# Performance work log

Hardware: AMD Instinct MI355X
Metric: run time of the kernel (lower is better)

The kernel has to match this reference:

```python
import jax, jax.numpy as jnp
import numpy as np

B, N, D = 8, 2048, 256
K = 3  # conv kernel size

def causal_conv(x, w, b):
    # x: [B, N, D] -> conv over seq with left replicate padding (causal)
    xc = jnp.transpose(x, (0, 2, 1))                       # [B, D, N]
    xc = jnp.pad(xc, ((0, 0), (0, 0), (K - 1, 0)), mode='edge')
    y = jax.lax.conv_general_dilated(
        xc, w, window_strides=(1,), padding='VALID',
        dimension_numbers=('NCH', 'OIH', 'NCH'))           # [B, Dout, N]
    y = y + b[None, :, None]
    return jnp.transpose(y, (0, 2, 1))                     # [B, N, Dout]

def setup_inputs() -> dict:
    key = jax.random.key(0)
    ks = jax.random.split(key, 5)
    query = jax.random.normal(ks[0], (B, N, D), dtype=jnp.float32)
    keys = jax.random.normal(ks[1], (B, N, D), dtype=jnp.float32)
    vals = jax.random.normal(ks[2], (B, N, D), dtype=jnp.float32)
    # causal mask [B, N, N]: attend to positions j <= i
    mask = jnp.broadcast_to(jnp.tril(jnp.ones((N, N), dtype=jnp.int32)), (B, N, N))
    conv_w = jax.random.normal(ks[3], (D, D, K), dtype=jnp.float32) * (1.0 / np.sqrt(D * K))
    conv_b = jnp.zeros((D,), dtype=jnp.float32)
    return {"query": query, "keys": keys, "vals": vals, "mask": mask,
            "conv_w": conv_w, "conv_b": conv_b}

def reference(query, keys, vals, mask, conv_w, conv_b):
    q = causal_conv(query, conv_w, conv_b)                 # [B, N, D]
    k = causal_conv(keys, conv_w, conv_b)                  # [B, N, D]
    # Euclidean pairwise distances: ||q_i - k_j||
    q2 = jnp.sum(q * q, axis=-1)                           # [B, N]
    k2 = jnp.sum(k * k, axis=-1)                           # [B, N]
    qk = jnp.einsum('bid,bjd->bij', q, k)                  # [B, N, N]
    d2 = jnp.maximum(q2[:, :, None] + k2[:, None, :] - 2.0 * qk, 0.0)
    distances = jnp.sqrt(d2)
    presoftmax = jnp.where(mask == 0, -jnp.inf, -distances)
    attn = jax.nn.softmax(presoftmax, axis=-1)             # [B, N, N]
    shifted_vals = jnp.roll(vals, shift=1, axis=1).at[:, 0, :].set(0.0)
    return jnp.einsum('bij,bjd->bid', attn, shifted_vals)  # [B, N, D]
```

## Files before the change

kernel.cpp:

```cpp
#include <hip/hip_runtime.h>

typedef _Float16 f16;
typedef _Float16 f16x4 __attribute__((ext_vector_type(4)));
typedef _Float16 f16x8 __attribute__((ext_vector_type(8)));
typedef float f32x4 __attribute__((ext_vector_type(4)));

#define NB 8
#define NS 2048
#define ND 256
#define NM (NB * NS)
#define LOG2E 1.44269504f


__device__ __forceinline__ int swzK(int row, int col) {
  return (((row) << 9) | ((col) << 1)) ^ (((row) & 7) << 4);
}

__global__ __launch_bounds__(256) void prep_kernel(
    const float* __restrict__ vals, const float* __restrict__ conv_w,
    f16* __restrict__ vT, f16* __restrict__ Wk) {
  int tid = threadIdx.x;
  if (blockIdx.x < 512) {
    __shared__ f16 Vl[32 * 256];
    int tile = blockIdx.x;
    for (int s = tid; s < 1024; s += 256) {
      int j = s >> 5, d0 = (s & 31) * 8;
      int g = tile * 32 + j;
      f16x8 h;
      if ((g & (NS - 1)) == 0) {
        for (int e = 0; e < 8; e++) h[e] = (f16)0.f;
      } else {
        const float* src = vals + (size_t)(g - 1) * ND + d0;
        f32x4 v0 = *(const f32x4*)src, v1 = *(const f32x4*)(src + 4);
        for (int e = 0; e < 4; e++) { h[e] = (f16)v0[e]; h[4 + e] = (f16)v1[e]; }
      }
      *(f16x8*)((char*)Vl + j * 512 + d0 * 2) = h;
    }
    __syncthreads();
    char* dst = (char*)vT + (size_t)tile * 16384;
    #pragma unroll
    for (int k = 0; k < 4; k++) {
      int ch = tid + k * 256;
      int lane = ch & 63;
      int d = ((ch >> 6) << 4) + (lane & 15);
      int g4c = lane >> 4;
      f16x8 h;
      #pragma unroll
      for (int js = 0; js < 2; js++)
        #pragma unroll
        for (int r = 0; r < 4; r++)
          h[js * 4 + r] = *(const f16*)((const char*)Vl + (js * 16 + 4 * g4c + r) * 512 + d * 2);
      *(f16x8*)(dst + ch * 16) = h;
    }
  } else {
    int e = (blockIdx.x - 512) * 256 + tid;
    if (e < 256 * 768) {
      int o = e / 768, kk = e - o * 768;
      int tap = kk >> 8, d = kk & 255;
      Wk[e] = (f16)conv_w[o * 768 + d * 3 + tap];
    }
  }
}

__global__ __launch_bounds__(256) void conv_kernel(
    const float* __restrict__ query, const float* __restrict__ keys,
    const float* __restrict__ bias, const f16* __restrict__ Wk,
    f16* __restrict__ qT, f16* __restrict__ kT,
    float* __restrict__ q2, float* __restrict__ k2) {
  __shared__ f16 Xl[66 * 256];
  __shared__ float red[4][64];
  int bid = blockIdx.x;
  int tens = bid >> 8;
  int tile = bid & 255;
  const float* X = tens ? keys : query;
  float* Y2 = tens ? k2 : q2;
  int base = tile * 64;
  int bstart = base & ~(NS - 1);
  int tid = threadIdx.x;
  for (int c = tid; c < 66 * 32; c += 256) {
    int row = c >> 5, d0 = (c & 31) * 8;
    int g = base - 2 + row; if (g < bstart) g = bstart;
    const float* src = X + (size_t)g * ND + d0;
    f32x4 v0 = *(const f32x4*)src, v1 = *(const f32x4*)(src + 4);
    f16x8 h;
    for (int e = 0; e < 4; e++) { h[e] = (f16)v0[e]; h[4 + e] = (f16)v1[e]; }
    *(f16x8*)((char*)Xl + swzK(row, d0)) = h;
  }
  __syncthreads();
  int lane = tid & 63, w = tid >> 6;
  int c16 = lane & 15, g4 = lane >> 4;
  f32x4 acc[4][4] = {};
  const f16* wbase = Wk + (size_t)(w * 64 + c16) * 768 + 8 * g4;
  f16x8 bcur[4], bnext[4];
  #pragma unroll
  for (int nt = 0; nt < 4; nt++) bcur[nt] = *(const f16x8*)(wbase + nt * 16 * 768);
  for (int ks = 0; ks < 24; ks++) {
    int kk0 = ks * 32;
    if (ks < 23) {
      #pragma unroll
      for (int nt = 0; nt < 4; nt++)
        bnext[nt] = *(const f16x8*)(wbase + nt * 16 * 768 + kk0 + 32);
    }
    int tap = kk0 >> 8, d0 = kk0 & 255;
    f16x8 afr[4];
    #pragma unroll
    for (int ms = 0; ms < 4; ms++)
      afr[ms] = *(const f16x8*)((const char*)Xl + swzK(ms * 16 + c16 + tap, d0 + 8 * g4));
    #pragma unroll
    for (int ms = 0; ms < 4; ms++)
      #pragma unroll
      for (int nt = 0; nt < 4; nt++)
        acc[ms][nt] = __builtin_amdgcn_mfma_f32_16x16x32_f16(afr[ms], bcur[nt], acc[ms][nt], 0, 0, 0);
    #pragma unroll
    for (int nt = 0; nt < 4; nt++) bcur[nt] = bnext[nt];
  }
  float bv[4];
  #pragma unroll
  for (int nt = 0; nt < 4; nt++) bv[nt] = bias[w * 64 + nt * 16 + c16];
  float rp[4][4];
  #pragma unroll
  for (int ms = 0; ms < 4; ms++)
    #pragma unroll
    for (int r = 0; r < 4; r++) {
      float s = 0.f;
      #pragma unroll
      for (int nt = 0; nt < 4; nt++) {
        float v = acc[ms][nt][r] + bv[nt];
        acc[ms][nt][r] = v;
        s += v * v;
      }
      rp[ms][r] = s;
    }
  #pragma unroll
  for (int off = 1; off < 16; off <<= 1)
    #pragma unroll
    for (int ms = 0; ms < 4; ms++)
      #pragma unroll
      for (int r = 0; r < 4; r++)
        rp[ms][r] += __shfl_xor(rp[ms][r], off, 64);
  if (c16 == 0)
    #pragma unroll
    for (int ms = 0; ms < 4; ms++)
      #pragma unroll
      for (int r = 0; r < 4; r++)
        red[w][ms * 16 + 4 * g4 + r] = rp[ms][r];
  __syncthreads();
  #pragma unroll
  for (int ms = 0; ms < 4; ms++)
    #pragma unroll
    for (int nt = 0; nt < 4; nt++)
      #pragma unroll
      for (int r = 0; r < 4; r++) {
        int row64 = ms * 16 + 4 * g4 + r;
        int col = w * 64 + nt * 16 + c16;
        int b;
        if (tens == 0)
          b = (row64 >> 4) * 8192 + (col >> 5) * 1024 + (row64 & 15) * 16
            + ((col >> 3) & 3) * 256 + (col & 7) * 2;
        else
          b = ((row64 >> 5) << 14) + (col >> 5) * 2048 + (((row64 >> 4) & 1) << 10)
            + (row64 & 15) * 16 + ((col >> 3) & 3) * 256 + (col & 7) * 2;
        b ^= ((b >> 7) & 7) << 4;
        *(f16*)((char*)Xl + b) = (f16)acc[ms][nt][r];
      }
  __syncthreads();
  char* dst = tens ? (char*)kT + ((size_t)(base >> 5) << 14)
                   : (char*)qT + ((size_t)(base >> 6) << 15);
  #pragma unroll
  for (int i = 0; i < 8; i++) {
    int b = tid * 128 + i * 16;
    f16x8 v = *(const f16x8*)((const char*)Xl + (b ^ (((b >> 7) & 7) << 4)));
    *(f16x8*)(dst + b) = v;
  }
  if (tid < 64)
    Y2[base + tid] = red[0][tid] + red[1][tid] + red[2][tid] + red[3][tid];
}

__global__ __launch_bounds__(64) void attn_kernel(
    const f16* __restrict__ qT, const f16* __restrict__ kT,
    const f16* __restrict__ vT, const float* __restrict__ q2,
    const float* __restrict__ k2, float* __restrict__ out,
    f16* __restrict__ partO, float2* __restrict__ partML, int TT, int S1) {
  int nwg = gridDim.x;
  int orig = blockIdx.x;
  int lg = (orig & 7) * (nwg >> 3) + (orig >> 3);
  int wq = lg & 3;
  int gc = lg >> 2;
  int ci = gc % S1, b = gc / S1;
  int itile = 0, pref = 0;
  for (int i = 0; i < 32; i++) {
    int cnt = (2 * (i + 1) + TT - 1) / TT;
    if (ci < pref + cnt) { itile = i; break; }
    pref += cnt;
  }
  int jc = ci - pref;
  int nc = (2 * (itile + 1) + TT - 1) / TT;
  int t0 = jc * TT;
  int t1 = min(t0 + TT, 2 * (itile + 1));
  int lane = threadIdx.x & 63;
  int c16 = lane & 15, g4 = lane >> 4;
  int rowbase = b * NS + itile * 64;
  int qrow = rowbase + wq * 16 + c16;
  int iglob = itile * 64 + wq * 16 + c16;
  f16x8 qf[8];
  {
    const char* qb = (const char*)qT + ((size_t)(b * 32 + itile) << 15)
                   + (wq << 13) + lane * 16;
    #pragma unroll
    for (int ks = 0; ks < 8; ks++)
      qf[ks] = *(const f16x8*)(qb + ks * 1024);
  }
  float q2v = q2[qrow];
  f32x4 o4[16] = {};
  float m_run = -1e30f, l_run = 0.f;
  const char* tb = (const char*)kT + ((size_t)(b * 64 + t0) << 14) + lane * 16;
  const char* vb = (const char*)vT + ((size_t)(b * 64 + t0) << 14) + lane * 16;
  for (int jt = t0; jt < t1; jt++) {
    int jb = b * NS + jt * 32;
    int jbs = jt * 32;
    f16x8 kf[8][2];
    #pragma unroll
    for (int ks = 0; ks < 8; ks++) {
      kf[ks][0] = *(const f16x8*)(tb + ks * 2048);
      kf[ks][1] = *(const f16x8*)(tb + ks * 2048 + 1024);
    }
    f32x4 s4[2] = {};
    #pragma unroll
    for (int ks = 0; ks < 8; ks++) {
      s4[0] = __builtin_amdgcn_mfma_f32_16x16x32_f16(kf[ks][0], qf[ks], s4[0], 0, 0, 0);
      s4[1] = __builtin_amdgcn_mfma_f32_16x16x32_f16(kf[ks][1], qf[ks], s4[1], 0, 0, 0);
    }
    f16x8 vv0[8];
    #pragma unroll
    for (int nt = 0; nt < 8; nt++)
      vv0[nt] = *(const f16x8*)(vb + nt * 1024);
    tb += 16384;
    float p[2][4];
    float mt = -1e30f;
    #pragma unroll
    for (int js = 0; js < 2; js++) {
      f32x4 k2v = *(const f32x4*)(k2 + jb + js * 16 + 4 * g4);
      #pragma unroll
      for (int r = 0; r < 4; r++) {
        int jsq = jbs + js * 16 + 4 * g4 + r;
        float d2 = fmaxf(q2v + k2v[r] - 2.f * s4[js][r], 0.f);
        float lg_ = -sqrtf(d2);
        if (jsq > iglob) lg_ = -1e30f;
        p[js][r] = lg_;
        mt = fmaxf(mt, lg_);
      }
    }
    mt = fmaxf(mt, __shfl_xor(mt, 16, 64));
    mt = fmaxf(mt, __shfl_xor(mt, 32, 64));
    if (!__all(mt <= m_run + 4.f)) {
      float m_new = fmaxf(m_run, mt);
      float scale = exp2f((m_run - m_new) * LOG2E);
      l_run *= scale;
      m_run = m_new;
      f32x4 sc;
      #pragma unroll
      for (int r = 0; r < 4; r++) sc[r] = __shfl(scale, 4 * g4 + r, 64);
      #pragma unroll
      for (int nt = 0; nt < 16; nt++)
        #pragma unroll
        for (int r = 0; r < 4; r++) o4[nt][r] *= sc[r];
    }
    f16x4 pa[2];
    #pragma unroll
    for (int js = 0; js < 2; js++)
      #pragma unroll
      for (int r = 0; r < 4; r++) {
        float pv = exp2f((p[js][r] - m_run) * LOG2E);
        l_run += pv;
        pa[js][r] = (f16)pv;
      }
    f16x8 vv1[8];
    #pragma unroll
    for (int nt = 0; nt < 8; nt++)
      vv1[nt] = *(const f16x8*)(vb + (8 + nt) * 1024);
    vb += 16384;
    #pragma unroll
    for (int nt = 0; nt < 8; nt++) {
      f16x4 vb0, vb1;
      #pragma unroll
      for (int r = 0; r < 4; r++) { vb0[r] = vv0[nt][r]; vb1[r] = vv0[nt][4 + r]; }
      o4[nt] = __builtin_amdgcn_mfma_f32_16x16x16f16(pa[0], vb0, o4[nt], 0, 0, 0);
      o4[nt] = __builtin_amdgcn_mfma_f32_16x16x16f16(pa[1], vb1, o4[nt], 0, 0, 0);
    }
    #pragma unroll
    for (int nt = 0; nt < 8; nt++) {
      f16x4 vb0, vb1;
      #pragma unroll
      for (int r = 0; r < 4; r++) { vb0[r] = vv1[nt][r]; vb1[r] = vv1[nt][4 + r]; }
      o4[8 + nt] = __builtin_amdgcn_mfma_f32_16x16x16f16(pa[0], vb0, o4[8 + nt], 0, 0, 0);
      o4[8 + nt] = __builtin_amdgcn_mfma_f32_16x16x16f16(pa[1], vb1, o4[8 + nt], 0, 0, 0);
    }
  }
  l_run += __shfl_xor(l_run, 16, 64);
  l_run += __shfl_xor(l_run, 32, 64);
  float inv = 1.f / l_run;
  f32x4 li;
  #pragma unroll
  for (int r = 0; r < 4; r++) li[r] = __shfl(inv, 4 * g4 + r, 64);
  if (nc == 1) {
    #pragma unroll
    for (int nt = 0; nt < 16; nt++)
      #pragma unroll
      for (int r = 0; r < 4; r++) {
        int irow = rowbase + wq * 16 + 4 * g4 + r;
        out[(size_t)irow * ND + nt * 16 + c16] = o4[nt][r] * li[r];
      }
  } else {
    if (g4 == 0)
      partML[(size_t)gc * 64 + wq * 16 + c16] = make_float2(m_run, l_run);
    char* pb = (char*)partO + ((size_t)gc << 15);
    #pragma unroll
    for (int q = 0; q < 8; q++) {
      f16x8 h;
      #pragma unroll
      for (int e = 0; e < 8; e++) {
        int nt = 2 * q + (e >> 2), r = e & 3;
        h[e] = (f16)(o4[nt][r] * li[r]);
      }
      *(f16x8*)(pb + q * 4096 + (wq * 64 + lane) * 16) = h;
    }
  }
}

__global__ __launch_bounds__(256) void combine_kernel(
    const f16* __restrict__ partO, const float2* __restrict__ partML,
    float* __restrict__ out, int TT, int S1) {
  int per = 32 - TT / 2;
  int b = blockIdx.x / per;
  int itile = TT / 2 + blockIdx.x % per;
  int nc = (2 * (itile + 1) + TT - 1) / TT;
  int pref = 0;
  for (int i = 0; i < itile; i++) pref += (2 * (i + 1) + TT - 1) / TT;
  size_t pbase = (size_t)b * S1 + pref;
  int tid = threadIdx.x, lane = tid & 63, w = tid >> 6;
  int c16 = lane & 15, g4 = lane >> 4;
  int mlrow = w * 16 + 4 * g4;
  float M[4] = {-1e30f, -1e30f, -1e30f, -1e30f};
  for (int c = 0; c < nc; ++c)
    #pragma unroll
    for (int r = 0; r < 4; r++)
      M[r] = fmaxf(M[r], partML[(pbase + c) * 64 + mlrow + r].x);
  float acc[64];
  #pragma unroll
  for (int i = 0; i < 64; i++) acc[i] = 0.f;
  float L[4] = {0.f, 0.f, 0.f, 0.f};
  for (int c = 0; c < nc; ++c) {
    float wcr[4];
    #pragma unroll
    for (int r = 0; r < 4; r++) {
      float2 ml = partML[(pbase + c) * 64 + mlrow + r];
      wcr[r] = ml.y * exp2f((ml.x - M[r]) * LOG2E);
      L[r] += wcr[r];
    }
    const char* pb = (const char*)partO + ((pbase + c) << 15);
    #pragma unroll
    for (int q = 0; q < 8; q++) {
      f16x8 v = *(const f16x8*)(pb + q * 4096 + tid * 16);
      #pragma unroll
      for (int e = 0; e < 8; e++) {
        int nt = 2 * q + (e >> 2), r = e & 3;
        acc[nt * 4 + r] += wcr[r] * (float)v[e];
      }
    }
  }
  #pragma unroll
  for (int r = 0; r < 4; r++) L[r] = 1.f / L[r];
  #pragma unroll
  for (int nt = 0; nt < 16; nt++)
    #pragma unroll
    for (int r = 0; r < 4; r++) {
      int irow = b * NS + itile * 64 + mlrow + r;
      out[(size_t)irow * ND + nt * 16 + c16] = acc[nt * 4 + r] * L[r];
    }
}

extern "C" void kernel_launch(void* const* d_in, const int* in_sizes, int n_in,
                              void* d_out, int out_size, void* d_ws, size_t ws_size,
                              hipStream_t stream) {
  const float* query  = (const float*)d_in[0];
  const float* keys   = (const float*)d_in[1];
  const float* vals   = (const float*)d_in[2];
  const float* conv_w = (const float*)d_in[4];
  const float* conv_b = (const float*)d_in[5];
  char* ws = (char*)d_ws;
  f16*   qT  = (f16*)(ws);
  f16*   kT  = (f16*)(ws + (size_t)8 * 1024 * 1024);
  f16*   vT  = (f16*)(ws + (size_t)16 * 1024 * 1024);
  f16*   Wk  = (f16*)(ws + (size_t)24 * 1024 * 1024);
  float* q2  = (float*)(ws + (size_t)24 * 1024 * 1024 + 512 * 1024);
  float* k2  = (float*)(ws + (size_t)24 * 1024 * 1024 + 576 * 1024);
  f16*   partO = (f16*)(ws + (size_t)25 * 1024 * 1024);
  float* out = (float*)d_out;

  const int TT = 8;
  int S1 = 0;
  for (int i = 0; i < 32; i++) S1 += (2 * (i + 1) + TT - 1) / TT;
  float2* partML = (float2*)(ws + (size_t)25 * 1024 * 1024 + (size_t)S1 * 8 * 32768);

  prep_kernel<<<1280, 256, 0, stream>>>(vals, conv_w, vT, Wk);
  conv_kernel<<<512, 256, 0, stream>>>(query, keys, conv_b, Wk, qT, kT, q2, k2);
  attn_kernel<<<8 * S1 * 4, 64, 0, stream>>>(qT, kT, vT, q2, k2, out,
                                             partO, partML, TT, S1);
  combine_kernel<<<8 * (32 - TT / 2), 256, 0, stream>>>(partO, partML, out, TT, S1);
}
```

Baseline: 114.0 us.

## Process two query subtiles per attention wave and pre-swizzle conv weights into fragment order

Each attention workgroup now handles two 16-row query subtiles instead of one. K and V fragments loaded from global memory are therefore reused across twice as many MFMAs, halving K/V traffic per output row, at the cost of doubled accumulator registers (two sets of 16 f32x4) and half as many workgroups. Separately, the conv weights are written in MFMA-fragment order so each lane in the conv kernel does one contiguous 16-byte load per fragment, and the prep grid shrinks to match. Higher register pressure may lower occupancy or cause spills.

```diff
diff --git a/kernel.cpp b/kernel.cpp
--- a/kernel.cpp
+++ b/kernel.cpp
@@ -18,7 +18,7 @@
 
 __global__ __launch_bounds__(256) void prep_kernel(
     const float* __restrict__ vals, const float* __restrict__ conv_w,
-    f16* __restrict__ vT, f16* __restrict__ Wk) {
+    f16* __restrict__ vT, f16* __restrict__ WkF) {
   int tid = threadIdx.x;
   if (blockIdx.x < 512) {
     __shared__ f16 Vl[32 * 256];
@@ -53,18 +53,26 @@
       *(f16x8*)(dst + ch * 16) = h;
     }
   } else {
-    int e = (blockIdx.x - 512) * 256 + tid;
-    if (e < 256 * 768) {
-      int o = e / 768, kk = e - o * 768;
-      int tap = kk >> 8, d = kk & 255;
-      Wk[e] = (f16)conv_w[o * 768 + d * 3 + tap];
+    int t = (blockIdx.x - 512) * 256 + tid;
+    if (t < 24576) {
+      int o = t / 96, kb = t - o * 96;
+      int k0 = kb * 8;
+      int ks = k0 >> 5, g4w = (k0 >> 3) & 3;
+      f16x8 h;
+      #pragma unroll
+      for (int e = 0; e < 8; e++) {
+        int k = k0 + e;
+        int tap = k >> 8, d = k & 255;
+        h[e] = (f16)conv_w[o * 768 + d * 3 + tap];
+      }
+      *(f16x8*)((char*)WkF + (size_t)((((o >> 4) * 24 + ks) * 64 + (o & 15) + 16 * g4w)) * 16) = h;
     }
   }
 }
 
 __global__ __launch_bounds__(256) void conv_kernel(
     const float* __restrict__ query, const float* __restrict__ keys,
-    const float* __restrict__ bias, const f16* __restrict__ Wk,
+    const float* __restrict__ bias, const f16* __restrict__ WkF,
     f16* __restrict__ qT, f16* __restrict__ kT,
     float* __restrict__ q2, float* __restrict__ k2) {
   __shared__ f16 Xl[66 * 256];
@@ -90,17 +98,17 @@
   int lane = tid & 63, w = tid >> 6;
   int c16 = lane & 15, g4 = lane >> 4;
   f32x4 acc[4][4] = {};
-  const f16* wbase = Wk + (size_t)(w * 64 + c16) * 768 + 8 * g4;
+  const char* wb = (const char*)WkF + ((size_t)(w * 4) * 24) * 1024 + lane * 16;
   f16x8 bcur[4], bnext[4];
   #pragma unroll
-  for (int nt = 0; nt < 4; nt++) bcur[nt] = *(const f16x8*)(wbase + nt * 16 * 768);
+  for (int nt = 0; nt < 4; nt++) bcur[nt] = *(const f16x8*)(wb + nt * 24 * 1024);
   for (int ks = 0; ks < 24; ks++) {
+    if (ks < 23) {
+      #pragma unroll
+      for (int nt = 0; nt < 4; nt++)
+        bnext[nt] = *(const f16x8*)(wb + (nt * 24 + ks + 1) * 1024);
+    }
     int kk0 = ks * 32;
-    if (ks < 23) {
-      #pragma unroll
-      for (int nt = 0; nt < 4; nt++)
-        bnext[nt] = *(const f16x8*)(wbase + nt * 16 * 768 + kk0 + 32);
-    }
     int tap = kk0 >> 8, d0 = kk0 & 255;
     f16x8 afr[4];
     #pragma unroll
@@ -184,8 +192,8 @@
   int nwg = gridDim.x;
   int orig = blockIdx.x;
   int lg = (orig & 7) * (nwg >> 3) + (orig >> 3);
-  int wq = lg & 3;
-  int gc = lg >> 2;
+  int wq2 = lg & 1;
+  int gc = lg >> 1;
   int ci = gc % S1, b = gc / S1;
   int itile = 0, pref = 0;
   for (int i = 0; i < 32; i++) {
@@ -200,19 +208,21 @@
   int lane = threadIdx.x & 63;
   int c16 = lane & 15, g4 = lane >> 4;
   int rowbase = b * NS + itile * 64;
-  int qrow = rowbase + wq * 16 + c16;
-  int iglob = itile * 64 + wq * 16 + c16;
-  f16x8 qf[8];
-  {
+  f16x8 qf[2][8];
+  float q2v[2];
+  int iglob[2];
+  #pragma unroll
+  for (int s = 0; s < 2; s++) {
     const char* qb = (const char*)qT + ((size_t)(b * 32 + itile) << 15)
-                   + (wq << 13) + lane * 16;
+                   + ((wq2 * 2 + s) << 13) + lane * 16;
     #pragma unroll
     for (int ks = 0; ks < 8; ks++)
-      qf[ks] = *(const f16x8*)(qb + ks * 1024);
-  }
-  float q2v = q2[qrow];
-  f32x4 o4[16] = {};
-  float m_run = -1e30f, l_run = 0.f;
+      qf[s][ks] = *(const f16x8*)(qb + ks * 1024);
+    q2v[s] = q2[rowbase + (wq2 * 2 + s) * 16 + c16];
+    iglob[s] = itile * 64 + (wq2 * 2 + s) * 16 + c16;
+  }
+  f32x4 o4[2][16] = {};
+  float m_run[2] = {-1e30f, -1e30f}, l_run[2] = {0.f, 0.f};
   const char* tb = (const char*)kT + ((size_t)(b * 64 + t0) << 14) + lane * 16;
   const char* vb = (const char*)vT + ((size_t)(b * 64 + t0) << 14) + lane * 16;
   for (int jt = t0; jt < t1; jt++) {
@@ -224,105 +234,122 @@
       kf[ks][0] = *(const f16x8*)(tb + ks * 2048);
       kf[ks][1] = *(const f16x8*)(tb + ks * 2048 + 1024);
     }
-    f32x4 s4[2] = {};
-    #pragma unroll
-    for (int ks = 0; ks < 8; ks++) {
-      s4[0] = __builtin_amdgcn_mfma_f32_16x16x32_f16(kf[ks][0], qf[ks], s4[0], 0, 0, 0);
-      s4[1] = __builtin_amdgcn_mfma_f32_16x16x32_f16(kf[ks][1], qf[ks], s4[1], 0, 0, 0);
-    }
-    f16x8 vv0[8];
+    tb += 16384;
+    f32x4 s4[2][2] = {};
+    #pragma unroll
+    for (int ks = 0; ks < 8; ks++)
+      #pragma unroll
+      for (int s = 0; s < 2; s++) {
+        s4[s][0] = __builtin_amdgcn_mfma_f32_16x16x32_f16(kf[ks][0], qf[s][ks], s4[s][0], 0, 0, 0);
+        s4[s][1] = __builtin_amdgcn_mfma_f32_16x16x32_f16(kf[ks][1], qf[s][ks], s4[s][1], 0, 0, 0);
+      }
+    f16x8 vv[8];
     #pragma unroll
     for (int nt = 0; nt < 8; nt++)
-      vv0[nt] = *(const f16x8*)(vb + nt * 1024);
-    tb += 16384;
-    float p[2][4];
-    float mt = -1e30f;
-    #pragma unroll
-    for (int js = 0; js < 2; js++) {
-      f32x4 k2v = *(const f32x4*)(k2 + jb + js * 16 + 4 * g4);
-      #pragma unroll
-      for (int r = 0; r < 4; r++) {
-        int jsq = jbs + js * 16 + 4 * g4 + r;
-        float d2 = fmaxf(q2v + k2v[r] - 2.f * s4[js][r], 0.f);
-        float lg_ = -sqrtf(d2);
-        if (jsq > iglob) lg_ = -1e30f;
-        p[js][r] = lg_;
-        mt = fmaxf(mt, lg_);
-      }
-    }
-    mt = fmaxf(mt, __shfl_xor(mt, 16, 64));
-    mt = fmaxf(mt, __shfl_xor(mt, 32, 64));
-    if (!__all(mt <= m_run + 4.f)) {
-      float m_new = fmaxf(m_run, mt);
-      float scale = exp2f((m_run - m_new) * LOG2E);
-      l_run *= scale;
-      m_run = m_new;
-      f32x4 sc;
-      #pragma unroll
-      for (int r = 0; r < 4; r++) sc[r] = __shfl(scale, 4 * g4 + r, 64);
-      #pragma unroll
-      for (int nt = 0; nt < 16; nt++)
-        #pragma unroll
-        for (int r = 0; r < 4; r++) o4[nt][r] *= sc[r];
-    }
-    f16x4 pa[2];
+      vv[nt] = *(const f16x8*)(vb + nt * 1024);
+    f32x4 k2v[2];
     #pragma unroll
     for (int js = 0; js < 2; js++)
-      #pragma unroll
-      for (int r = 0; r < 4; r++) {
-        float pv = exp2f((p[js][r] - m_run) * LOG2E);
-        l_run += pv;
-        pa[js][r] = (f16)pv;
-      }
-    f16x8 vv1[8];
-    #pragma unroll
-    for (int nt = 0; nt < 8; nt++)
-      vv1[nt] = *(const f16x8*)(vb + (8 + nt) * 1024);
-    vb += 16384;
+      k2v[js] = *(const f32x4*)(k2 + jb + js * 16 + 4 * g4);
+    f16x4 pa[2][2];
+    #pragma unroll
+    for (int s = 0; s < 2; s++) {
+      float p[2][4];
+      float mt = -1e30f;
+      #pragma unroll
+      for (int js = 0; js < 2; js++)
+        #pragma unroll
+        for (int r = 0; r < 4; r++) {
+          int jsq = jbs + js * 16 + 4 * g4 + r;
+          float d2 = fmaxf(q2v[s] + k2v[js][r] - 2.f * s4[s][js][r], 0.f);
+          float lg_ = -sqrtf(d2);
+          if (jsq > iglob[s]) lg_ = -1e30f;
+          p[js][r] = lg_;
+          mt = fmaxf(mt, lg_);
+        }
+      mt = fmaxf(mt, __shfl_xor(mt, 16, 64));
+      mt = fmaxf(mt, __shfl_xor(mt, 32, 64));
+      if (!__all(mt <= m_run[s] + 4.f)) {
+        float m_new = fmaxf(m_run[s], mt);
+        float scale = exp2f((m_run[s] - m_new) * LOG2E);
+        l_run[s] *= scale;
+        m_run[s] = m_new;
+        f32x4 sc;
+        #pragma unroll
+        for (int r = 0; r < 4; r++) sc[r] = __shfl(scale, 4 * g4 + r, 64);
+        #pragma unroll
+        for (int nt = 0; nt < 16; nt++)
+          #pragma unroll
+          for (int r = 0; r < 4; r++) o4[s][nt][r] *= sc[r];
+      }
+      #pragma unroll
+      for (int js = 0; js < 2; js++)
+        #pragma unroll
+        for (int r = 0; r < 4; r++) {
+          float pv = exp2f((p[js][r] - m_run[s]) * LOG2E);
+          l_run[s] += pv;
+          pa[s][js][r] = (f16)pv;
+        }
+    }
     #pragma unroll
     for (int nt = 0; nt < 8; nt++) {
       f16x4 vb0, vb1;
       #pragma unroll
-      for (int r = 0; r < 4; r++) { vb0[r] = vv0[nt][r]; vb1[r] = vv0[nt][4 + r]; }
-      o4[nt] = __builtin_amdgcn_mfma_f32_16x16x16f16(pa[0], vb0, o4[nt], 0, 0, 0);
-      o4[nt] = __builtin_amdgcn_mfma_f32_16x16x16f16(pa[1], vb1, o4[nt], 0, 0, 0);
-    }
+      for (int r = 0; r < 4; r++) { vb0[r] = vv[nt][r]; vb1[r] = vv[nt][4 + r]; }
+      #pragma unroll
+      for (int s = 0; s < 2; s++) {
+        o4[s][nt] = __builtin_amdgcn_mfma_f32_16x16x16f16(pa[s][0], vb0, o4[s][nt], 0, 0, 0);
+        o4[s][nt] = __builtin_amdgcn_mfma_f32_16x16x16f16(pa[s][1], vb1, o4[s][nt], 0, 0, 0);
+      }
+    }
+    #pragma unroll
+    for (int nt = 0; nt < 8; nt++)
+      vv[nt] = *(const f16x8*)(vb + (8 + nt) * 1024);
+    vb += 16384;
     #pragma unroll
     for (int nt = 0; nt < 8; nt++) {
       f16x4 vb0, vb1;
       #pragma unroll
-      for (int r = 0; r < 4; r++) { vb0[r] = vv1[nt][r]; vb1[r] = vv1[nt][4 + r]; }
-      o4[8 + nt] = __builtin_amdgcn_mfma_f32_16x16x16f16(pa[0], vb0, o4[8 + nt], 0, 0, 0);
-      o4[8 + nt] = __builtin_amdgcn_mfma_f32_16x16x16f16(pa[1], vb1, o4[8 + nt], 0, 0, 0);
-    }
-  }
-  l_run += __shfl_xor(l_run, 16, 64);
-  l_run += __shfl_xor(l_run, 32, 64);
-  float inv = 1.f / l_run;
-  f32x4 li;
-  #pragma unroll
-  for (int r = 0; r < 4; r++) li[r] = __shfl(inv, 4 * g4 + r, 64);
-  if (nc == 1) {
-    #pragma unroll
-    for (int nt = 0; nt < 16; nt++)
-      #pragma unroll
-      for (int r = 0; r < 4; r++) {
-        int irow = rowbase + wq * 16 + 4 * g4 + r;
-        out[(size_t)irow * ND + nt * 16 + c16] = o4[nt][r] * li[r];
-      }
-  } else {
-    if (g4 == 0)
-      partML[(size_t)gc * 64 + wq * 16 + c16] = make_float2(m_run, l_run);
-    char* pb = (char*)partO + ((size_t)gc << 15);
-    #pragma unroll
-    for (int q = 0; q < 8; q++) {
-      f16x8 h;
-      #pragma unroll
-      for (int e = 0; e < 8; e++) {
-        int nt = 2 * q + (e >> 2), r = e & 3;
-        h[e] = (f16)(o4[nt][r] * li[r]);
-      }
-      *(f16x8*)(pb + q * 4096 + (wq * 64 + lane) * 16) = h;
+      for (int r = 0; r < 4; r++) { vb0[r] = vv[nt][r]; vb1[r] = vv[nt][4 + r]; }
+      #pragma unroll
+      for (int s = 0; s < 2; s++) {
+        o4[s][8 + nt] = __builtin_amdgcn_mfma_f32_16x16x16f16(pa[s][0], vb0, o4[s][8 + nt], 0, 0, 0);
+        o4[s][8 + nt] = __builtin_amdgcn_mfma_f32_16x16x16f16(pa[s][1], vb1, o4[s][8 + nt], 0, 0, 0);
+      }
+    }
+  }
+  #pragma unroll
+  for (int s = 0; s < 2; s++) {
+    float l = l_run[s];
+    l += __shfl_xor(l, 16, 64);
+    l += __shfl_xor(l, 32, 64);
+    l_run[s] = l;
+    float inv = 1.f / l;
+    f32x4 li;
+    #pragma unroll
+    for (int r = 0; r < 4; r++) li[r] = __shfl(inv, 4 * g4 + r, 64);
+    if (nc == 1) {
+      #pragma unroll
+      for (int nt = 0; nt < 16; nt++)
+        #pragma unroll
+        for (int r = 0; r < 4; r++) {
+          int irow = rowbase + (wq2 * 2 + s) * 16 + 4 * g4 + r;
+          out[(size_t)irow * ND + nt * 16 + c16] = o4[s][nt][r] * li[r];
+        }
+    } else {
+      if (g4 == 0)
+        partML[(size_t)gc * 64 + (wq2 * 2 + s) * 16 + c16] = make_float2(m_run[s], l_run[s]);
+      char* pb = (char*)partO + ((size_t)gc << 15);
+      #pragma unroll
+      for (int q = 0; q < 8; q++) {
+        f16x8 h;
+        #pragma unroll
+        for (int e = 0; e < 8; e++) {
+          int nt = 2 * q + (e >> 2), r = e & 3;
+          h[e] = (f16)(o4[s][nt][r] * li[r]);
+        }
+        *(f16x8*)(pb + q * 4096 + ((wq2 * 2 + s) * 64 + lane) * 16) = h;
+      }
     }
   }
 }
@@ -391,7 +418,7 @@
   f16*   qT  = (f16*)(ws);
   f16*   kT  = (f16*)(ws + (size_t)8 * 1024 * 1024);
   f16*   vT  = (f16*)(ws + (size_t)16 * 1024 * 1024);
-  f16*   Wk  = (f16*)(ws + (size_t)24 * 1024 * 1024);
+  f16*   WkF = (f16*)(ws + (size_t)24 * 1024 * 1024);
   float* q2  = (float*)(ws + (size_t)24 * 1024 * 1024 + 512 * 1024);
   float* k2  = (float*)(ws + (size_t)24 * 1024 * 1024 + 576 * 1024);
   f16*   partO = (f16*)(ws + (size_t)25 * 1024 * 1024);
@@ -402,9 +429,9 @@
   for (int i = 0; i < 32; i++) S1 += (2 * (i + 1) + TT - 1) / TT;
   float2* partML = (float2*)(ws + (size_t)25 * 1024 * 1024 + (size_t)S1 * 8 * 32768);
 
-  prep_kernel<<<1280, 256, 0, stream>>>(vals, conv_w, vT, Wk);
-  conv_kernel<<<512, 256, 0, stream>>>(query, keys, conv_b, Wk, qT, kT, q2, k2);
-  attn_kernel<<<8 * S1 * 4, 64, 0, stream>>>(qT, kT, vT, q2, k2, out,
+  prep_kernel<<<608, 256, 0, stream>>>(vals, conv_w, vT, WkF);
+  conv_kernel<<<512, 256, 0, stream>>>(query, keys, conv_b, WkF, qT, kT, q2, k2);
+  attn_kernel<<<8 * S1 * 2, 64, 0, stream>>>(qT, kT, vT, q2, k2, out,
                                              partO, partML, TT, S1);
   combine_kernel<<<8 * (32 - TT / 2), 256, 0, stream>>>(partO, partML, out, TT, S1);
 }
```

Result: slower. 130.8 us (+14.7%).

## Pre-swizzle conv weights into MFMA fragment layout and trim attention register footprint

Applied to the files above, without the earlier changes.

The prep kernel now writes conv weights as 8-wide f16 chunks arranged in MFMA fragment order. Each lane of the conv kernel can then load its B fragment with one contiguous 16-byte read, instead of strided per-row reads, and fewer prep blocks are launched. The attention kernel loads K fragments in two halves and reuses a single V register buffer for both halves of the output columns. This cuts peak VGPR use, which may raise occupancy, at the cost of less load-ahead latency hiding.

```diff
diff --git a/kernel.cpp b/kernel.cpp
--- a/kernel.cpp
+++ b/kernel.cpp
@@ -18,7 +18,7 @@
 
 __global__ __launch_bounds__(256) void prep_kernel(
     const float* __restrict__ vals, const float* __restrict__ conv_w,
-    f16* __restrict__ vT, f16* __restrict__ Wk) {
+    f16* __restrict__ vT, f16* __restrict__ WkF) {
   int tid = threadIdx.x;
   if (blockIdx.x < 512) {
     __shared__ f16 Vl[32 * 256];
@@ -53,18 +53,26 @@
       *(f16x8*)(dst + ch * 16) = h;
     }
   } else {
-    int e = (blockIdx.x - 512) * 256 + tid;
-    if (e < 256 * 768) {
-      int o = e / 768, kk = e - o * 768;
-      int tap = kk >> 8, d = kk & 255;
-      Wk[e] = (f16)conv_w[o * 768 + d * 3 + tap];
+    int t = (blockIdx.x - 512) * 256 + tid;
+    if (t < 24576) {
+      int o = t / 96, kb = t - o * 96;
+      int k0 = kb * 8;
+      int ks = k0 >> 5, g4w = (k0 >> 3) & 3;
+      f16x8 h;
+      #pragma unroll
+      for (int e = 0; e < 8; e++) {
+        int k = k0 + e;
+        int tap = k >> 8, d = k & 255;
+        h[e] = (f16)conv_w[o * 768 + d * 3 + tap];
+      }
+      *(f16x8*)((char*)WkF + (size_t)((((o >> 4) * 24 + ks) * 64 + (o & 15) + 16 * g4w)) * 16) = h;
     }
   }
 }
 
 __global__ __launch_bounds__(256) void conv_kernel(
     const float* __restrict__ query, const float* __restrict__ keys,
-    const float* __restrict__ bias, const f16* __restrict__ Wk,
+    const float* __restrict__ bias, const f16* __restrict__ WkF,
     f16* __restrict__ qT, f16* __restrict__ kT,
     float* __restrict__ q2, float* __restrict__ k2) {
   __shared__ f16 Xl[66 * 256];
@@ -90,17 +98,17 @@
   int lane = tid & 63, w = tid >> 6;
   int c16 = lane & 15, g4 = lane >> 4;
   f32x4 acc[4][4] = {};
-  const f16* wbase = Wk + (size_t)(w * 64 + c16) * 768 + 8 * g4;
+  const char* wb = (const char*)WkF + ((size_t)(w * 4) * 24) * 1024 + lane * 16;
   f16x8 bcur[4], bnext[4];
   #pragma unroll
-  for (int nt = 0; nt < 4; nt++) bcur[nt] = *(const f16x8*)(wbase + nt * 16 * 768);
+  for (int nt = 0; nt < 4; nt++) bcur[nt] = *(const f16x8*)(wb + nt * 24 * 1024);
   for (int ks = 0; ks < 24; ks++) {
+    if (ks < 23) {
+      #pragma unroll
+      for (int nt = 0; nt < 4; nt++)
+        bnext[nt] = *(const f16x8*)(wb + (nt * 24 + ks + 1) * 1024);
+    }
     int kk0 = ks * 32;
-    if (ks < 23) {
-      #pragma unroll
-      for (int nt = 0; nt < 4; nt++)
-        bnext[nt] = *(const f16x8*)(wbase + nt * 16 * 768 + kk0 + 32);
-    }
     int tap = kk0 >> 8, d0 = kk0 & 255;
     f16x8 afr[4];
     #pragma unroll
@@ -218,22 +226,25 @@
   for (int jt = t0; jt < t1; jt++) {
     int jb = b * NS + jt * 32;
     int jbs = jt * 32;
-    f16x8 kf[8][2];
-    #pragma unroll
-    for (int ks = 0; ks < 8; ks++) {
-      kf[ks][0] = *(const f16x8*)(tb + ks * 2048);
-      kf[ks][1] = *(const f16x8*)(tb + ks * 2048 + 1024);
-    }
     f32x4 s4[2] = {};
     #pragma unroll
-    for (int ks = 0; ks < 8; ks++) {
-      s4[0] = __builtin_amdgcn_mfma_f32_16x16x32_f16(kf[ks][0], qf[ks], s4[0], 0, 0, 0);
-      s4[1] = __builtin_amdgcn_mfma_f32_16x16x32_f16(kf[ks][1], qf[ks], s4[1], 0, 0, 0);
-    }
-    f16x8 vv0[8];
+    for (int h = 0; h < 2; h++) {
+      f16x8 kf[4][2];
+      #pragma unroll
+      for (int ks = 0; ks < 4; ks++) {
+        kf[ks][0] = *(const f16x8*)(tb + (h * 4 + ks) * 2048);
+        kf[ks][1] = *(const f16x8*)(tb + (h * 4 + ks) * 2048 + 1024);
+      }
+      #pragma unroll
+      for (int ks = 0; ks < 4; ks++) {
+        s4[0] = __builtin_amdgcn_mfma_f32_16x16x32_f16(kf[ks][0], qf[h * 4 + ks], s4[0], 0, 0, 0);
+        s4[1] = __builtin_amdgcn_mfma_f32_16x16x32_f16(kf[ks][1], qf[h * 4 + ks], s4[1], 0, 0, 0);
+      }
+    }
+    f16x8 vv[8];
     #pragma unroll
     for (int nt = 0; nt < 8; nt++)
-      vv0[nt] = *(const f16x8*)(vb + nt * 1024);
+      vv[nt] = *(const f16x8*)(vb + nt * 1024);
     tb += 16384;
     float p[2][4];
     float mt = -1e30f;
@@ -274,24 +285,23 @@
         l_run += pv;
         pa[js][r] = (f16)pv;
       }
-    f16x8 vv1[8];
-    #pragma unroll
-    for (int nt = 0; nt < 8; nt++)
-      vv1[nt] = *(const f16x8*)(vb + (8 + nt) * 1024);
-    vb += 16384;
     #pragma unroll
     for (int nt = 0; nt < 8; nt++) {
       f16x4 vb0, vb1;
       #pragma unroll
-      for (int r = 0; r < 4; r++) { vb0[r] = vv0[nt][r]; vb1[r] = vv0[nt][4 + r]; }
+      for (int r = 0; r < 4; r++) { vb0[r] = vv[nt][r]; vb1[r] = vv[nt][4 + r]; }
       o4[nt] = __builtin_amdgcn_mfma_f32_16x16x16f16(pa[0], vb0, o4[nt], 0, 0, 0);
       o4[nt] = __builtin_amdgcn_mfma_f32_16x16x16f16(pa[1], vb1, o4[nt], 0, 0, 0);
     }
     #pragma unroll
+    for (int nt = 0; nt < 8; nt++)
+      vv[nt] = *(const f16x8*)(vb + (8 + nt) * 1024);
+    vb += 16384;
+    #pragma unroll
     for (int nt = 0; nt < 8; nt++) {
       f16x4 vb0, vb1;
       #pragma unroll
-      for (int r = 0; r < 4; r++) { vb0[r] = vv1[nt][r]; vb1[r] = vv1[nt][4 + r]; }
+      for (int r = 0; r < 4; r++) { vb0[r] = vv[nt][r]; vb1[r] = vv[nt][4 + r]; }
       o4[8 + nt] = __builtin_amdgcn_mfma_f32_16x16x16f16(pa[0], vb0, o4[8 + nt], 0, 0, 0);
       o4[8 + nt] = __builtin_amdgcn_mfma_f32_16x16x16f16(pa[1], vb1, o4[8 + nt], 0, 0, 0);
     }
@@ -391,7 +401,7 @@
   f16*   qT  = (f16*)(ws);
   f16*   kT  = (f16*)(ws + (size_t)8 * 1024 * 1024);
   f16*   vT  = (f16*)(ws + (size_t)16 * 1024 * 1024);
-  f16*   Wk  = (f16*)(ws + (size_t)24 * 1024 * 1024);
+  f16*   WkF = (f16*)(ws + (size_t)24 * 1024 * 1024);
   float* q2  = (float*)(ws + (size_t)24 * 1024 * 1024 + 512 * 1024);
   float* k2  = (float*)(ws + (size_t)24 * 1024 * 1024 + 576 * 1024);
   f16*   partO = (f16*)(ws + (size_t)25 * 1024 * 1024);
@@ -402,8 +412,8 @@
   for (int i = 0; i < 32; i++) S1 += (2 * (i + 1) + TT - 1) / TT;
   float2* partML = (float2*)(ws + (size_t)25 * 1024 * 1024 + (size_t)S1 * 8 * 32768);
 
-  prep_kernel<<<1280, 256, 0, stream>>>(vals, conv_w, vT, Wk);
-  conv_kernel<<<512, 256, 0, stream>>>(query, keys, conv_b, Wk, qT, kT, q2, k2);
+  prep_kernel<<<608, 256, 0, stream>>>(vals, conv_w, vT, WkF);
+  conv_kernel<<<512, 256, 0, stream>>>(query, keys, conv_b, WkF, qT, kT, q2, k2);
   attn_kernel<<<8 * S1 * 4, 64, 0, stream>>>(qT, kT, vT, q2, k2, out,
                                              partO, partML, TT, S1);
   combine_kernel<<<8 * (32 - TT / 2), 256, 0, stream>>>(partO, partML, out, TT, S1);
```

After: 107.7 us. -5.5%, faster.
